# Kernel optimization log

Hardware: AMD Instinct MI355X
Metric: run time of the kernel (lower is better)

Reference implementation:

```python
import jax, jax.numpy as jnp
import numpy as np

D_MODEL = 1024
N_HEAD = 16
D_K = 64
D_V = 64
LN_EPS = 1e-5


def setup_inputs() -> dict:
    key = jax.random.key(0)
    ks = jax.random.split(key, 12)
    B, S = 4, 2048
    s = 1.0 / np.sqrt(D_MODEL)
    inp = {
        "q": jax.random.normal(ks[0], (B, S, D_MODEL), jnp.float32),
        "k": jax.random.normal(ks[1], (B, S, D_MODEL), jnp.float32),
        "v": jax.random.normal(ks[2], (B, S, D_MODEL), jnp.float32),
        "mask": jnp.ones((B, S, S), jnp.int32),
        "w_q": jax.random.normal(ks[3], (D_MODEL, N_HEAD * D_K), jnp.float32) * s,
        "b_q": jnp.zeros((N_HEAD * D_K,), jnp.float32),
        "w_k": jax.random.normal(ks[4], (D_MODEL, N_HEAD * D_K), jnp.float32) * s,
        "b_k": jnp.zeros((N_HEAD * D_K,), jnp.float32),
        "w_v": jax.random.normal(ks[5], (D_MODEL, N_HEAD * D_V), jnp.float32) * s,
        "b_v": jnp.zeros((N_HEAD * D_V,), jnp.float32),
        "w_fc": jax.random.normal(ks[6], (N_HEAD * D_V, D_MODEL), jnp.float32) * s,
        "b_fc": jnp.zeros((D_MODEL,), jnp.float32),
        "ln_g": jnp.ones((D_MODEL,), jnp.float32),
        "ln_b": jnp.zeros((D_MODEL,), jnp.float32),
    }
    return inp


def reference(q, k, v, mask, w_q, b_q, w_k, b_k, w_v, b_v, w_fc, b_fc, ln_g, ln_b):
    B, Sq, _ = q.shape
    Sk = k.shape[1]
    residual = q
    # QKV projections -> [B, H, S, d]
    qh = (q @ w_q + b_q).reshape(B, Sq, N_HEAD, D_K).transpose(0, 2, 1, 3)
    kh = (k @ w_k + b_k).reshape(B, Sk, N_HEAD, D_K).transpose(0, 2, 1, 3)
    vh = (v @ w_v + b_v).reshape(B, Sk, N_HEAD, D_V).transpose(0, 2, 1, 3)
    temp = jnp.sqrt(jnp.asarray(D_K, qh.dtype))
    scores = jnp.einsum("bhqd,bhkd->bhqk", qh / temp, kh)
    scores = jnp.where(mask[:, None, :, :] == 0, jnp.asarray(-1e9, scores.dtype), scores)
    attn = jax.nn.softmax(scores, axis=-1)  # dropout is identity in eval
    out = jnp.einsum("bhqk,bhkd->bhqd", attn, vh)
    out = out.transpose(0, 2, 1, 3).reshape(B, Sq, N_HEAD * D_V)
    out = out @ w_fc + b_fc  # output proj (dropout identity)
    x = out + residual
    mu = jnp.mean(x, axis=-1, keepdims=True)
    var = jnp.mean(jnp.square(x - mu), axis=-1, keepdims=True)
    y = (x - mu) * jax.lax.rsqrt(var + LN_EPS) * ln_g + ln_b
    return (y, attn)
```

## Files before the change

kernel.cpp:

```cpp
#include <hip/hip_runtime.h>
#include <cstdint>
#include <cstddef>

#define DM 1024
#define HN 16
#define DH 64
#define BB 4
#define SS 2048
#define MM (BB * SS)

typedef __bf16 bf16;
typedef bf16 bf16x8 __attribute__((ext_vector_type(8)));
typedef bf16 bf16x4 __attribute__((ext_vector_type(4)));
typedef float f32x4 __attribute__((ext_vector_type(4)));
typedef int i32x4 __attribute__((ext_vector_type(4)));

__device__ __forceinline__ f32x4 mfma16(bf16x8 a, bf16x8 b, f32x4 c) {
  return __builtin_amdgcn_mfma_f32_16x16x32_bf16(a, b, c, 0, 0, 0);
}

typedef __attribute__((address_space(3))) void lds_void_t;
typedef __attribute__((address_space(1))) void glob_void_t;

__device__ __forceinline__ void gload16(const void* g, void* l) {
  __builtin_amdgcn_global_load_lds((const glob_void_t*)g, (lds_void_t*)l, 16, 0, 0);
}

__global__ __launch_bounds__(256) void mask_bitsT(const int* __restrict__ mask,
                                                  unsigned int* __restrict__ mT) {
  int qt = blockIdx.x, b = blockIdx.y;
  int col0 = threadIdx.x * 8;
  unsigned int m[8] = {0, 0, 0, 0, 0, 0, 0, 0};
  const int* mp = mask + ((size_t)b * SS + qt * 32) * SS + col0;
  for (int r = 0; r < 32; ++r) {
    i32x4 a = *(const i32x4*)(mp + (size_t)r * SS);
    i32x4 c = *(const i32x4*)(mp + (size_t)r * SS + 4);
#pragma unroll
    for (int i = 0; i < 4; ++i) {
      m[i] |= (unsigned int)(a[i] != 0) << r;
      m[4 + i] |= (unsigned int)(c[i] != 0) << r;
    }
  }
#pragma unroll
  for (int i = 0; i < 8; ++i)
    mT[((size_t)b * 64 + qt) * SS + col0 + i] = m[i];
}

__global__ __launch_bounds__(256) void cvt3(const float* __restrict__ q,
                                            const float* __restrict__ k,
                                            const float* __restrict__ v,
                                            bf16* __restrict__ dst) {
  int which = blockIdx.y;
  const float* in = which == 0 ? q : which == 1 ? k : v;
  bf16* out = dst + (size_t)which * MM * DM;
  int i = (blockIdx.x * 256 + threadIdx.x) * 8;
  f32x4 a = *(const f32x4*)(in + i);
  f32x4 b = *(const f32x4*)(in + i + 4);
  bf16x8 o;
  o[0] = (bf16)a[0]; o[1] = (bf16)a[1]; o[2] = (bf16)a[2]; o[3] = (bf16)a[3];
  o[4] = (bf16)b[0]; o[5] = (bf16)b[1]; o[6] = (bf16)b[2]; o[7] = (bf16)b[3];
  *(bf16x8*)(out + i) = o;
}

__global__ __launch_bounds__(256) void wtrans4(const float* __restrict__ w_q,
                                               const float* __restrict__ w_k,
                                               const float* __restrict__ w_v,
                                               const float* __restrict__ w_fc,
                                               bf16* __restrict__ WT) {
  int p = blockIdx.z;
  const float* W = p == 0 ? w_q : p == 1 ? w_k : p == 2 ? w_v : w_fc;
  bf16* out = WT + (size_t)p * DM * DM;
  __shared__ float t[32][33];
  int n0 = blockIdx.x * 32, k0 = blockIdx.y * 32;
  int tid = threadIdx.x;
  int r = tid >> 3, c = (tid & 7) * 4;
  f32x4 v = *(const f32x4*)&W[(size_t)(k0 + r) * DM + n0 + c];
  t[r][c] = v[0]; t[r][c + 1] = v[1]; t[r][c + 2] = v[2]; t[r][c + 3] = v[3];
  __syncthreads();
  bf16x4 o;
#pragma unroll
  for (int i = 0; i < 4; ++i) o[i] = (bf16)t[c + i][r];
  *(bf16x4*)&out[(size_t)(n0 + r) * DM + k0 + c] = o;
}

__global__ __launch_bounds__(256) void gemm_qkv(const bf16* __restrict__ Abase,
                                                const bf16* __restrict__ Bt,
                                                const float* __restrict__ b_q,
                                                const float* __restrict__ b_k,
                                                const float* __restrict__ b_v,
                                                bf16* __restrict__ qhh,
                                                bf16* __restrict__ khh,
                                                bf16* __restrict__ vhT) {
  constexpr int K = DM;
  __shared__ bf16 Ab[128 * 32];
  __shared__ bf16 Bb[128 * 32];
  int tid = threadIdx.x, wave = tid >> 6, lane = tid & 63;
  int bm = blockIdx.x * 128, bn = blockIdx.y * 128;
  int proj = bn >> 10;
  const bf16* A = Abase + (size_t)proj * MM * DM;
  const float* bias = proj == 0 ? b_q : proj == 1 ? b_k : b_v;
  int wr = (wave >> 1) * 64, wc = (wave & 1) * 64;
  int fr = lane & 15, kg8 = (lane >> 4) * 8;
  f32x4 acc[4][4] = {};
  int arow = tid >> 2, acol = (tid & 3) * 8;
  const bf16* Ag0 = A + (size_t)(bm + arow) * K + acol;
  const bf16* Ag1 = Ag0 + (size_t)64 * K;
  const bf16* Bg0 = Bt + (size_t)(bn + arow) * K + acol;
  const bf16* Bg1 = Bg0 + (size_t)64 * K;
  char* la = (char*)Ab + wave * 1024;
  char* lb = (char*)Bb + wave * 1024;
  for (int k0 = 0; k0 < K; k0 += 32) {
    __syncthreads();
    gload16(Ag0 + k0, la);
    gload16(Ag1 + k0, la + 4096);
    gload16(Bg0 + k0, lb);
    gload16(Bg1 + k0, lb + 4096);
    asm volatile("s_waitcnt vmcnt(0)" ::: "memory");
    __syncthreads();
    bf16x8 af[4], bfr[4];
#pragma unroll
    for (int m = 0; m < 4; ++m)
      af[m] = *(const bf16x8*)&Ab[(wr + m * 16 + fr) * 32 + kg8];
#pragma unroll
    for (int n = 0; n < 4; ++n)
      bfr[n] = *(const bf16x8*)&Bb[(wc + n * 16 + fr) * 32 + kg8];
#pragma unroll
    for (int m = 0; m < 4; ++m)
#pragma unroll
      for (int n = 0; n < 4; ++n) acc[m][n] = mfma16(af[m], bfr[n], acc[m][n]);
  }
  int b = bm >> 11;
#pragma unroll
  for (int m = 0; m < 4; ++m)
#pragma unroll
    for (int n = 0; n < 4; ++n) {
      int c = bn + wc + n * 16 + fr;
      int lc = c & 1023;
      float bv = bias[lc];
      int h = lc >> 6, d = lc & 63;
      int r0 = bm + wr + m * 16 + (lane >> 4) * 4;
      int s0 = r0 & (SS - 1);
      if (proj == 2) {
        bf16x4 o;
#pragma unroll
        for (int j = 0; j < 4; ++j) o[j] = (bf16)(acc[m][n][j] + bv);
        *(bf16x4*)&vhT[(size_t)(b * HN + h) * (SS * DH) +
                       (size_t)(s0 >> 5) * (DH * 32) + d * 32 + (s0 & 31)] = o;
      } else {
        bf16* dst = proj == 0 ? qhh : khh;
        float sc = proj == 0 ? 0.125f : 1.f;
#pragma unroll
        for (int j = 0; j < 4; ++j) {
          float v = (acc[m][n][j] + bv) * sc;
          dst[(size_t)(b * HN + h) * (SS * DH) + (size_t)(s0 + j) * DH + d] =
              (bf16)v;
        }
      }
    }
}

__global__ __launch_bounds__(256) void gemm_out(const bf16* __restrict__ A,
                                                const bf16* __restrict__ Bt,
                                                const float* __restrict__ bias,
                                                const float* __restrict__ resid,
                                                float* __restrict__ out) {
  constexpr int K = DM;
  __shared__ bf16 Ab[128 * 32];
  __shared__ bf16 Bb[128 * 32];
  int tid = threadIdx.x, wave = tid >> 6, lane = tid & 63;
  int bm = blockIdx.x * 128, bn = blockIdx.y * 128;
  int wr = (wave >> 1) * 64, wc = (wave & 1) * 64;
  int fr = lane & 15, kg8 = (lane >> 4) * 8;
  f32x4 acc[4][4] = {};
  int arow = tid >> 2, acol = (tid & 3) * 8;
  const bf16* Ag0 = A + (size_t)(bm + arow) * K + acol;
  const bf16* Ag1 = Ag0 + (size_t)64 * K;
  const bf16* Bg0 = Bt + (size_t)(bn + arow) * K + acol;
  const bf16* Bg1 = Bg0 + (size_t)64 * K;
  char* la = (char*)Ab + wave * 1024;
  char* lb = (char*)Bb + wave * 1024;
  for (int k0 = 0; k0 < K; k0 += 32) {
    __syncthreads();
    gload16(Ag0 + k0, la);
    gload16(Ag1 + k0, la + 4096);
    gload16(Bg0 + k0, lb);
    gload16(Bg1 + k0, lb + 4096);
    asm volatile("s_waitcnt vmcnt(0)" ::: "memory");
    __syncthreads();
    bf16x8 af[4], bfr[4];
#pragma unroll
    for (int m = 0; m < 4; ++m)
      af[m] = *(const bf16x8*)&Ab[(wr + m * 16 + fr) * 32 + kg8];
#pragma unroll
    for (int n = 0; n < 4; ++n)
      bfr[n] = *(const bf16x8*)&Bb[(wc + n * 16 + fr) * 32 + kg8];
#pragma unroll
    for (int m = 0; m < 4; ++m)
#pragma unroll
      for (int n = 0; n < 4; ++n) acc[m][n] = mfma16(af[m], bfr[n], acc[m][n]);
  }
#pragma unroll
  for (int m = 0; m < 4; ++m)
#pragma unroll
    for (int n = 0; n < 4; ++n) {
      int c = bn + wc + n * 16 + fr;
      float bv = bias[c];
#pragma unroll
      for (int j = 0; j < 4; ++j) {
        int r = bm + wr + m * 16 + (lane >> 4) * 4 + j;
        size_t idx = (size_t)r * DM + c;
        out[idx] = acc[m][n][j] + bv + resid[idx];
      }
    }
}

__global__ __launch_bounds__(1024, 4) void attn_kernel(
    const bf16* __restrict__ qh, const bf16* __restrict__ kh,
    const bf16* __restrict__ vhT, const unsigned int* __restrict__ mT,
    float* __restrict__ attn_out, bf16* __restrict__ ctx) {
  extern __shared__ char smem[];
  float* invp = (float*)(smem + 32 * 4096);
  int tid = threadIdx.x, wave = tid >> 6, lane = tid & 63;
  int fid = (blockIdx.x & 7) * 512 + (blockIdx.x >> 3);
  int bh = fid >> 6, qt = fid & 63;
  int b = bh >> 4, h = bh & 15;
  int q0 = qt * 32;
  const bf16* qbase = qh + ((size_t)bh * SS + q0) * DH;
  const bf16* kbase = kh + (size_t)bh * SS * DH;
  const bf16* vbase = vhT + (size_t)bh * SS * DH;
  const unsigned int* mTb = mT + ((size_t)b * 64 + qt) * SS;
  int fr = lane & 15, kg = lane >> 4;

  bf16x8 qa0 = *(const bf16x8*)&qbase[(size_t)fr * DH + kg * 8];
  bf16x8 qa1 = *(const bf16x8*)&qbase[(size_t)fr * DH + 32 + kg * 8];
  bf16x8 qb0 = *(const bf16x8*)&qbase[(size_t)(16 + fr) * DH + kg * 8];
  bf16x8 qb1 = *(const bf16x8*)&qbase[(size_t)(16 + fr) * DH + 32 + kg * 8];

  {
    int sw = wave * 128;
    bf16x8 kb0[8], kb1[8];
    auto kload = [&](int g) {
      const bf16* kp = kbase + (size_t)(sw + g * 16 + fr) * DH + kg * 8;
      kb0[g & 7] = *(const bf16x8*)kp;
      kb1[g & 7] = *(const bf16x8*)(kp + 32);
    };
#pragma unroll
    for (int g = 0; g < 4; ++g) kload(g);
#pragma unroll
    for (int g = 0; g < 8; ++g) {
      if (g < 4) kload(g + 4);
      f32x4 aa = {0.f, 0.f, 0.f, 0.f};
      f32x4 ab = {0.f, 0.f, 0.f, 0.f};
      aa = mfma16(qa0, kb0[g & 7], aa);
      aa = mfma16(qa1, kb1[g & 7], aa);
      ab = mfma16(qb0, kb0[g & 7], ab);
      ab = mfma16(qb1, kb1[g & 7], ab);
      int col = sw + g * 16 + fr;
      unsigned int bits = mTb[col];
      int slot = col >> 3, within = col & 7;
#pragma unroll
      for (int j = 0; j < 4; ++j) {
        int ra = kg * 4 + j;
        int rb_ = ra + 16;
        float fa = ((bits >> ra) & 1u) ? __expf(aa[j]) : 0.f;
        float fb = ((bits >> rb_) & 1u) ? __expf(ab[j]) : 0.f;
        *(bf16*)(smem + ra * 4096 + ((slot ^ ra) << 4) + within * 2) = (bf16)fa;
        *(bf16*)(smem + rb_ * 4096 + ((slot ^ rb_) << 4) + within * 2) = (bf16)fb;
      }
    }
  }
  __syncthreads();

  {
    int row = wave * 2 + (lane >> 5);
    int la = lane & 31;
    char* rbase = smem + row * 4096;
    float sum = 0.f;
#pragma unroll
    for (int it = 0; it < 8; ++it) {
      int slot = la + it * 32;
      bf16x8 e = *(const bf16x8*)(rbase + ((slot ^ row) << 4));
#pragma unroll
      for (int i = 0; i < 8; ++i) sum += (float)e[i];
    }
#pragma unroll
    for (int off = 1; off < 32; off <<= 1) sum += __shfl_xor(sum, off);
    if (la == 0) invp[row] = 1.f / sum;
  }
  __syncthreads();

  if (wave < 8) {
    int rb = wave >> 2, dq = wave & 3;
    f32x4 cacc = {0.f, 0.f, 0.f, 0.f};
    const bf16* vtile = vbase + (dq * 16 + fr) * 32 + kg * 8;
    int prow_row = rb * 16 + fr;
    char* prow = smem + prow_row * 4096;
    bf16x8 vb[8], pb[8];
    auto pvload = [&](int kk) {
      vb[kk & 7] = *(const bf16x8*)&vtile[(size_t)kk * (DH * 32)];
      int slotA = kk * 4 + kg;
      pb[kk & 7] = *(const bf16x8*)(prow + ((slotA ^ prow_row) << 4));
    };
    pvload(0);
    pvload(1);
    pvload(2);
    pvload(3);
    __builtin_amdgcn_s_setprio(1);
#pragma unroll
    for (int kk = 0; kk < 64; ++kk) {
      if (kk < 60) pvload(kk + 4);
      cacc = mfma16(pb[kk & 7], vb[kk & 7], cacc);
    }
    __builtin_amdgcn_s_setprio(0);
#pragma unroll
    for (int j = 0; j < 4; ++j) {
      int row = rb * 16 + kg * 4 + j;
      float v = cacc[j] * invp[row];
      ctx[((size_t)b * SS + q0 + row) * DM + h * DH + dq * 16 + fr] = (bf16)v;
    }
  } else {
    int t = (wave - 8) * 64 + lane;
    int slot = t >> 1, halfoff = (t & 1) * 8;
    float* outb = attn_out + ((size_t)bh * SS + q0) * SS;
#pragma unroll 4
    for (int r = 0; r < 32; ++r) {
      bf16x4 e = *(const bf16x4*)(smem + r * 4096 + ((slot ^ r) << 4) + halfoff);
      float inv = invp[r];
      f32x4 u = {(float)e[0] * inv, (float)e[1] * inv, (float)e[2] * inv,
                 (float)e[3] * inv};
      *(f32x4*)(outb + (size_t)r * SS + t * 4) = u;
    }
  }
}

__global__ __launch_bounds__(256) void ln_k(float* __restrict__ x,
                                            const float* __restrict__ g,
                                            const float* __restrict__ bln) {
  int r = blockIdx.x, tid = threadIdx.x;
  f32x4 v = *(const f32x4*)&x[(size_t)r * DM + tid * 4];
  float s = v[0] + v[1] + v[2] + v[3];
  float s2 = v[0] * v[0] + v[1] * v[1] + v[2] * v[2] + v[3] * v[3];
#pragma unroll
  for (int off = 32; off; off >>= 1) {
    s += __shfl_down(s, off);
    s2 += __shfl_down(s2, off);
  }
  __shared__ float rs_[4], rs2_[4];
  int wave = tid >> 6, lane = tid & 63;
  if (lane == 0) {
    rs_[wave] = s;
    rs2_[wave] = s2;
  }
  __syncthreads();
  s = rs_[0] + rs_[1] + rs_[2] + rs_[3];
  s2 = rs2_[0] + rs2_[1] + rs2_[2] + rs2_[3];
  float mu = s * (1.f / DM);
  float var = s2 * (1.f / DM) - mu * mu;
  float rstd = rsqrtf(var + 1e-5f);
  f32x4 gg = *(const f32x4*)&g[tid * 4];
  f32x4 bb = *(const f32x4*)&bln[tid * 4];
  f32x4 o;
#pragma unroll
  for (int i = 0; i < 4; ++i) o[i] = (v[i] - mu) * rstd * gg[i] + bb[i];
  *(f32x4*)&x[(size_t)r * DM + tid * 4] = o;
}

extern "C" void kernel_launch(void* const* d_in, const int* in_sizes, int n_in,
                              void* d_out, int out_size, void* d_ws,
                              size_t ws_size, hipStream_t stream) {
  const float* q = (const float*)d_in[0];
  const float* k = (const float*)d_in[1];
  const float* v = (const float*)d_in[2];
  const int* mask = (const int*)d_in[3];
  const float* w_q = (const float*)d_in[4];
  const float* b_q = (const float*)d_in[5];
  const float* w_k = (const float*)d_in[6];
  const float* b_k = (const float*)d_in[7];
  const float* w_v = (const float*)d_in[8];
  const float* b_v = (const float*)d_in[9];
  const float* w_fc = (const float*)d_in[10];
  const float* b_fc = (const float*)d_in[11];
  const float* ln_g = (const float*)d_in[12];
  const float* ln_b = (const float*)d_in[13];

  float* y = (float*)d_out;
  float* attn_out = (float*)d_out + (size_t)MM * DM;

  char* w = (char*)d_ws;
  const size_t actN = (size_t)MM * DM;
  bf16* qkv_bf = (bf16*)w;  w += 3 * actN * 2;
  bf16* wT = (bf16*)w;      w += (size_t)4 * DM * DM * 2;
  bf16* qhh = (bf16*)w;     w += actN * 2;
  bf16* khh = (bf16*)w;     w += actN * 2;
  bf16* vhT = (bf16*)w;     w += actN * 2;
  bf16* ctx = (bf16*)w;     w += actN * 2;
  unsigned int* mT = (unsigned int*)w;  w += (size_t)BB * 64 * SS * 4;

  mask_bitsT<<<dim3(SS / 32, BB), 256, 0, stream>>>(mask, mT);
  cvt3<<<dim3(4096, 3), 256, 0, stream>>>(q, k, v, qkv_bf);
  wtrans4<<<dim3(DM / 32, DM / 32, 4), 256, 0, stream>>>(w_q, w_k, w_v, w_fc, wT);
  gemm_qkv<<<dim3(MM / 128, 3072 / 128), 256, 0, stream>>>(
      qkv_bf, wT, b_q, b_k, b_v, qhh, khh, vhT);
  hipFuncSetAttribute((const void*)attn_kernel,
                      hipFuncAttributeMaxDynamicSharedMemorySize, 131200);
  attn_kernel<<<4096, 1024, 131200, stream>>>(
      qhh, khh, vhT, mT, attn_out, ctx);
  gemm_out<<<dim3(MM / 128, DM / 128), 256, 0, stream>>>(
      ctx, wT + (size_t)3 * DM * DM, b_fc, q, y);
  ln_k<<<MM, 256, 0, stream>>>(y, ln_g, ln_b);
}
```

Measured before the change: 645.1 us.

## Shrink attention tile to 16 query rows with 512-thread blocks

The attention kernel now handles 16 query rows per block instead of 32, using 512 threads and half the LDS (about 64KB), with twice as many blocks. Each wave covers 256 key columns for the QK stage. The mask bits are shifted to pick the right half, and the attn writeout now stores 8 values per thread. The aim is more resident blocks per CU and less LDS per block, at the cost of reloading K and V twice as often per query.

Result: slower. 695.9 us (+7.9%).

```diff
diff --git a/kernel.cpp b/kernel.cpp
--- a/kernel.cpp
+++ b/kernel.cpp
@@ -214,30 +214,29 @@
     }
 }
 
-__global__ __launch_bounds__(1024, 4) void attn_kernel(
+__global__ __launch_bounds__(512, 4) void attn_kernel(
     const bf16* __restrict__ qh, const bf16* __restrict__ kh,
     const bf16* __restrict__ vhT, const unsigned int* __restrict__ mT,
     float* __restrict__ attn_out, bf16* __restrict__ ctx) {
   extern __shared__ char smem[];
-  float* invp = (float*)(smem + 32 * 4096);
+  float* invp = (float*)(smem + 16 * 4096);
   int tid = threadIdx.x, wave = tid >> 6, lane = tid & 63;
-  int fid = (blockIdx.x & 7) * 512 + (blockIdx.x >> 3);
-  int bh = fid >> 6, qt = fid & 63;
+  int fid = (blockIdx.x & 7) * 1024 + (blockIdx.x >> 3);
+  int bh = fid >> 7, qt = fid & 127;
   int b = bh >> 4, h = bh & 15;
-  int q0 = qt * 32;
+  int q0 = qt * 16;
   const bf16* qbase = qh + ((size_t)bh * SS + q0) * DH;
   const bf16* kbase = kh + (size_t)bh * SS * DH;
   const bf16* vbase = vhT + (size_t)bh * SS * DH;
-  const unsigned int* mTb = mT + ((size_t)b * 64 + qt) * SS;
+  const unsigned int* mTb = mT + ((size_t)b * 64 + (qt >> 1)) * SS;
+  int rsh = (qt & 1) * 16;
   int fr = lane & 15, kg = lane >> 4;
 
   bf16x8 qa0 = *(const bf16x8*)&qbase[(size_t)fr * DH + kg * 8];
   bf16x8 qa1 = *(const bf16x8*)&qbase[(size_t)fr * DH + 32 + kg * 8];
-  bf16x8 qb0 = *(const bf16x8*)&qbase[(size_t)(16 + fr) * DH + kg * 8];
-  bf16x8 qb1 = *(const bf16x8*)&qbase[(size_t)(16 + fr) * DH + 32 + kg * 8];
 
   {
-    int sw = wave * 128;
+    int sw = wave * 256;
     bf16x8 kb0[8], kb1[8];
     auto kload = [&](int g) {
       const bf16* kp = kbase + (size_t)(sw + g * 16 + fr) * DH + kg * 8;
@@ -247,25 +246,19 @@
 #pragma unroll
     for (int g = 0; g < 4; ++g) kload(g);
 #pragma unroll
-    for (int g = 0; g < 8; ++g) {
-      if (g < 4) kload(g + 4);
+    for (int g = 0; g < 16; ++g) {
+      if (g < 12) kload(g + 4);
       f32x4 aa = {0.f, 0.f, 0.f, 0.f};
-      f32x4 ab = {0.f, 0.f, 0.f, 0.f};
       aa = mfma16(qa0, kb0[g & 7], aa);
       aa = mfma16(qa1, kb1[g & 7], aa);
-      ab = mfma16(qb0, kb0[g & 7], ab);
-      ab = mfma16(qb1, kb1[g & 7], ab);
       int col = sw + g * 16 + fr;
-      unsigned int bits = mTb[col];
+      unsigned int bits = mTb[col] >> rsh;
       int slot = col >> 3, within = col & 7;
 #pragma unroll
       for (int j = 0; j < 4; ++j) {
         int ra = kg * 4 + j;
-        int rb_ = ra + 16;
         float fa = ((bits >> ra) & 1u) ? __expf(aa[j]) : 0.f;
-        float fb = ((bits >> rb_) & 1u) ? __expf(ab[j]) : 0.f;
         *(bf16*)(smem + ra * 4096 + ((slot ^ ra) << 4) + within * 2) = (bf16)fa;
-        *(bf16*)(smem + rb_ * 4096 + ((slot ^ rb_) << 4) + within * 2) = (bf16)fb;
       }
     }
   }
@@ -289,17 +282,16 @@
   }
   __syncthreads();
 
-  if (wave < 8) {
-    int rb = wave >> 2, dq = wave & 3;
+  if (wave < 4) {
+    int dq = wave;
     f32x4 cacc = {0.f, 0.f, 0.f, 0.f};
     const bf16* vtile = vbase + (dq * 16 + fr) * 32 + kg * 8;
-    int prow_row = rb * 16 + fr;
-    char* prow = smem + prow_row * 4096;
+    char* prow = smem + fr * 4096;
     bf16x8 vb[8], pb[8];
     auto pvload = [&](int kk) {
       vb[kk & 7] = *(const bf16x8*)&vtile[(size_t)kk * (DH * 32)];
       int slotA = kk * 4 + kg;
-      pb[kk & 7] = *(const bf16x8*)(prow + ((slotA ^ prow_row) << 4));
+      pb[kk & 7] = *(const bf16x8*)(prow + ((slotA ^ fr) << 4));
     };
     pvload(0);
     pvload(1);
@@ -314,21 +306,23 @@
     __builtin_amdgcn_s_setprio(0);
 #pragma unroll
     for (int j = 0; j < 4; ++j) {
-      int row = rb * 16 + kg * 4 + j;
+      int row = kg * 4 + j;
       float v = cacc[j] * invp[row];
       ctx[((size_t)b * SS + q0 + row) * DM + h * DH + dq * 16 + fr] = (bf16)v;
     }
   } else {
-    int t = (wave - 8) * 64 + lane;
-    int slot = t >> 1, halfoff = (t & 1) * 8;
+    int t = (wave - 4) * 64 + lane;
     float* outb = attn_out + ((size_t)bh * SS + q0) * SS;
 #pragma unroll 4
-    for (int r = 0; r < 32; ++r) {
-      bf16x4 e = *(const bf16x4*)(smem + r * 4096 + ((slot ^ r) << 4) + halfoff);
+    for (int r = 0; r < 16; ++r) {
+      bf16x8 e = *(const bf16x8*)(smem + r * 4096 + ((t ^ r) << 4));
       float inv = invp[r];
-      f32x4 u = {(float)e[0] * inv, (float)e[1] * inv, (float)e[2] * inv,
-                 (float)e[3] * inv};
-      *(f32x4*)(outb + (size_t)r * SS + t * 4) = u;
+      f32x4 u0 = {(float)e[0] * inv, (float)e[1] * inv, (float)e[2] * inv,
+                  (float)e[3] * inv};
+      f32x4 u1 = {(float)e[4] * inv, (float)e[5] * inv, (float)e[6] * inv,
+                  (float)e[7] * inv};
+      *(f32x4*)(outb + (size_t)r * SS + t * 8) = u0;
+      *(f32x4*)(outb + (size_t)r * SS + t * 8 + 4) = u1;
     }
   }
 }
@@ -402,8 +396,8 @@
   gemm_qkv<<<dim3(MM / 128, 3072 / 128), 256, 0, stream>>>(
       qkv_bf, wT, b_q, b_k, b_v, qhh, khh, vhT);
   hipFuncSetAttribute((const void*)attn_kernel,
-                      hipFuncAttributeMaxDynamicSharedMemorySize, 131200);
-  attn_kernel<<<4096, 1024, 131200, stream>>>(
+                      hipFuncAttributeMaxDynamicSharedMemorySize, 65600);
+  attn_kernel<<<8192, 512, 65600, stream>>>(
       qhh, khh, vhT, mT, attn_out, ctx);
   gemm_out<<<dim3(MM / 128, DM / 128), 256, 0, stream>>>(
       ctx, wT + (size_t)3 * DM * DM, b_fc, q, y);
```
